# Kernel optimization log

Measured on AMD Instinct MI355X. Metric: run time of the kernel, lower is better.

Reference implementation:

```python
import jax, jax.numpy as jnp
import numpy as np

N_NODES = 50000
N_EDGES = 1600000
D_IN = 128
D_HID = 256


def gcn_conv(x, edge_index, W, b, n_nodes):
    # PyG GCNConv: linear transform, add self-loops, symmetric deg^-1/2 normalization,
    # scatter-sum aggregation, then bias.
    h = x @ W                                             # [N, out]
    src, dst = edge_index[0], edge_index[1]
    loop = jnp.arange(n_nodes, dtype=src.dtype)
    src = jnp.concatenate([src, loop])
    dst = jnp.concatenate([dst, loop])
    deg = jax.ops.segment_sum(jnp.ones_like(dst, x.dtype), dst, num_segments=n_nodes)
    dinv = jnp.where(deg > 0, jax.lax.rsqrt(deg), 0.0)    # deg^-1/2, guard isolated nodes
    norm = dinv[src] * dinv[dst]                          # [E+N]
    msg = norm[:, None] * h[src]                          # gather + scale
    out = jax.ops.segment_sum(msg, dst, num_segments=n_nodes)  # scatter-sum
    return out + b


def setup_inputs() -> dict:
    key = jax.random.key(0)
    k_x, k_e, k_w1, k_b1, k_w2, k_b2 = jax.random.split(key, 6)
    x = jax.random.normal(k_x, (N_NODES, D_IN), dtype=jnp.float32)
    edge_index = jax.random.randint(k_e, (2, N_EDGES), 0, N_NODES, dtype=jnp.int64)
    s = 1.0 / np.sqrt(D_IN)
    W1 = jax.random.uniform(k_w1, (D_IN, D_HID), jnp.float32, -s, s)
    b1 = jnp.zeros((D_HID,), jnp.float32)
    s2 = 1.0 / np.sqrt(D_HID)
    W2 = jax.random.uniform(k_w2, (D_HID, D_IN), jnp.float32, -s2, s2)
    b2 = jnp.zeros((D_IN,), jnp.float32)
    return {"x": x, "edge_index": edge_index, "W1": W1, "b1": b1, "W2": W2, "b2": b2}


def reference(x, edge_index, W1, b1, W2, b2):
    h = gcn_conv(x, edge_index, W1, b1, N_NODES)   # conv1 (hetero sum over 1 edge type)
    h = jax.nn.relu(h)
    out = gcn_conv(h, edge_index, W2, b2, N_NODES) # conv2 -> x_dict['asset']
    return out
```

## Files before the change

### kernel.cpp

```cpp
#include <hip/hip_runtime.h>

#define N_NODES 50000
#define N_EDGES 1600000
#define D_IN 128
#define D_HID 256

#define NBKT 391
#define BCAP 6144
#define CHUNK 4096

typedef short bh8 __attribute__((ext_vector_type(8)));
typedef float f32x4 __attribute__((ext_vector_type(4)));

__device__ inline unsigned int f2_to_bf16x2(float a, float b) {
    unsigned int ua = __float_as_uint(a);
    ua = (ua + 0x7FFFu + ((ua >> 16) & 1u)) >> 16;
    unsigned int ub = __float_as_uint(b);
    ub = (ub + 0x7FFFu + ((ub >> 16) & 1u)) >> 16;
    return ua | (ub << 16);
}
__device__ inline unsigned short f_to_bf16(float a) {
    unsigned int ua = __float_as_uint(a);
    return (unsigned short)((ua + 0x7FFFu + ((ua >> 16) & 1u)) >> 16);
}
__device__ inline float2 bf16x2_to_f2(unsigned int p) {
    float2 r;
    r.x = __uint_as_float(p << 16);
    r.y = __uint_as_float(p & 0xFFFF0000u);
    return r;
}

__global__ __launch_bounds__(256) void bin_kernel(
        const int* __restrict__ src, const int* __restrict__ dst,
        int* __restrict__ bcur, unsigned int* __restrict__ binned, int E) {
    __shared__ unsigned int staged[CHUNK];
    __shared__ unsigned int sorted[CHUNK];
    __shared__ int hist[NBKT], lbase[NBKT], gbase[NBKT];
    __shared__ int sc[256];
    const int tid = threadIdx.x;
    for (int i = tid; i < NBKT; i += 256) hist[i] = 0;
    __syncthreads();
    const int cbase = blockIdx.x * CHUNK;
    const int n = min(CHUNK, E - cbase);
    for (int i = tid; i < n; i += 256) {
        int s = src[cbase + i], d = dst[cbase + i];
        staged[i] = ((unsigned)s << 16) | (unsigned)d;
        atomicAdd(&hist[d >> 7], 1);
    }
    __syncthreads();
    int v0 = (2 * tid     < NBKT) ? hist[2 * tid]     : 0;
    int v1 = (2 * tid + 1 < NBKT) ? hist[2 * tid + 1] : 0;
    sc[tid] = v0 + v1;
    __syncthreads();
    for (int off = 1; off < 256; off <<= 1) {
        int a = (tid >= off) ? sc[tid - off] : 0;
        __syncthreads();
        sc[tid] += a;
        __syncthreads();
    }
    int pairex = sc[tid] - (v0 + v1);
    if (2 * tid < NBKT) {
        lbase[2 * tid] = pairex;
        gbase[2 * tid] = v0 ? atomicAdd(&bcur[2 * tid], v0) : 0;
        hist[2 * tid] = 0;
    }
    if (2 * tid + 1 < NBKT) {
        lbase[2 * tid + 1] = pairex + v0;
        gbase[2 * tid + 1] = v1 ? atomicAdd(&bcur[2 * tid + 1], v1) : 0;
        hist[2 * tid + 1] = 0;
    }
    __syncthreads();
    for (int i = tid; i < n; i += 256) {
        unsigned r = staged[i];
        int b = (r & 0xFFFF) >> 7;
        sorted[lbase[b] + atomicAdd(&hist[b], 1)] = r;
    }
    __syncthreads();
    for (int j = tid; j < n; j += 256) {
        unsigned r = sorted[j];
        int b = (r & 0xFFFF) >> 7;
        binned[(size_t)b * BCAP + gbase[b] + (j - lbase[b])] = r;
    }
}

__global__ __launch_bounds__(512) void scanB(const int* __restrict__ bcur,
                                             int* __restrict__ brow) {
    __shared__ int sc[512];
    const int tid = threadIdx.x;
    int v = (tid < NBKT) ? bcur[tid] : 0;
    sc[tid] = v;
    __syncthreads();
    for (int off = 1; off < 512; off <<= 1) {
        int a = (tid >= off) ? sc[tid - off] : 0;
        __syncthreads();
        sc[tid] += a;
        __syncthreads();
    }
    if (tid < NBKT) brow[tid] = sc[tid] - v;
}

__global__ __launch_bounds__(256) void count_kernel(
        const unsigned int* __restrict__ binned, const int* __restrict__ bcur,
        const int* __restrict__ brow, int* __restrict__ deg,
        float* __restrict__ dinv, int* __restrict__ rowptr, int nNodes) {
    __shared__ int h[128], sc[128];
    const int b = blockIdx.x, tid = threadIdx.x;
    if (tid < 128) h[tid] = 0;
    __syncthreads();
    const int cnt = bcur[b];
    for (int j = tid; j < cnt; j += 256)
        atomicAdd(&h[binned[(size_t)b * BCAP + j] & 127], 1);
    __syncthreads();
    if (tid < 128) {
        sc[tid] = h[tid];
    }
    __syncthreads();
    for (int off = 1; off < 128; off <<= 1) {
        int a = (tid < 128 && tid >= off) ? sc[tid - off] : 0;
        __syncthreads();
        if (tid < 128) sc[tid] += a;
        __syncthreads();
    }
    int node = b * 128 + tid;
    if (tid < 128 && node < nNodes) {
        int d0 = h[tid];
        deg[node] = d0;
        dinv[node] = rsqrtf((float)(d0 + 1));
        rowptr[node] = brow[b] + sc[tid] - d0;
    }
}

__global__ __launch_bounds__(256) void place_kernel(
        const unsigned int* __restrict__ binned, const int* __restrict__ bcur,
        const int* __restrict__ rowptr, const float* __restrict__ dinv,
        unsigned short* __restrict__ eS, float* __restrict__ eW, int nNodes) {
    __shared__ int cur[128];
    __shared__ float sdinv[128];
    __shared__ unsigned short recS[BCAP];
    const int b = blockIdx.x, tid = threadIdx.x;
    const int nbase = b * 128;
    const int regionBase = rowptr[nbase];
    if (tid < 128) {
        int node = nbase + tid;
        cur[tid] = (node < nNodes) ? (rowptr[node] - regionBase) : 0;
        sdinv[tid] = (node < nNodes) ? dinv[node] : 0.0f;
    }
    __syncthreads();
    int cnt = bcur[b];
    if (cnt <= BCAP) {
        for (int j = tid; j < cnt; j += 256) {
            unsigned r = binned[(size_t)b * BCAP + j];
            int dl = r & 127;
            int s = r >> 16;
            int p = atomicAdd(&cur[dl], 1);
            recS[p] = (unsigned short)s;
            eW[regionBase + p] = dinv[s] * sdinv[dl];
        }
        __syncthreads();
        for (int j = tid; j < cnt; j += 256)
            eS[regionBase + j] = recS[j];
    } else {
        for (int j = tid; j < cnt; j += 256) {
            unsigned r = binned[(size_t)b * BCAP + j];
            int dl = r & 127;
            int s = r >> 16;
            int p = atomicAdd(&cur[dl], 1);
            eS[regionBase + p] = (unsigned short)s;
            eW[regionBase + p] = dinv[s] * sdinv[dl];
        }
    }
}

__global__ __launch_bounds__(256) void cvt_bf16(const float4* __restrict__ in,
                                                uint2* __restrict__ out, int n4) {
    int i = blockIdx.x * blockDim.x + threadIdx.x;
    if (i < n4) {
        float4 v = in[i];
        out[i] = make_uint2(f2_to_bf16x2(v.x, v.y), f2_to_bf16x2(v.z, v.w));
    }
}

__global__ __launch_bounds__(256) void cvtT_both(const float* __restrict__ W1,
                                                 const float* __restrict__ W2,
                                                 unsigned short* __restrict__ W1T,
                                                 unsigned short* __restrict__ W2T) {
    int t = blockIdx.x * blockDim.x + threadIdx.x;
    const int SZ = D_IN * D_HID;
    if (t < SZ) {
        int n = t / D_IN, k = t - n * D_IN;
        W1T[t] = f_to_bf16(W1[(size_t)k * D_HID + n]);
    } else if (t < 2 * SZ) {
        int u = t - SZ;
        int n = u / D_HID, k = u - n * D_HID;
        W2T[u] = f_to_bf16(W2[(size_t)k * D_IN + n]);
    }
}

template<bool OUT_BF16>
__global__ __launch_bounds__(256) void gather_agg_bf16(
        const uint2* __restrict__ hb2,
        const unsigned short* __restrict__ eS,
        const float* __restrict__ eW,
        const int* __restrict__ rowptr, const int* __restrict__ deg,
        const float* __restrict__ dinv, const float* __restrict__ bias,
        void* __restrict__ out, int n) {
    const int lane = threadIdx.x & 63;
    const int node = blockIdx.x * 4 + (threadIdx.x >> 6);
    if (node >= n) return;
    const int hl = lane & 31;
    const int odd = (lane >> 5) & 1;
    const int start = rowptr[node];
    const int cnt = deg[node];
    const float dn = dinv[node];

    float4 acc = make_float4(0.f, 0.f, 0.f, 0.f);
    if (!odd) {
        uint2 hv = hb2[(size_t)node * 32 + hl];
        float2 a = bf16x2_to_f2(hv.x), b = bf16x2_to_f2(hv.y);
        float w = dn * dn;
        acc.x = w * a.x; acc.y = w * a.y; acc.z = w * b.x; acc.w = w * b.y;
    }

    for (int c0 = 0; c0 < cnt; c0 += 64) {
        int m = min(64, cnt - c0);
        int   es = (lane < m) ? (int)eS[start + c0 + lane] : 0;
        float ws = (lane < m) ? eW[start + c0 + lane] : 0.0f;
        int steps = (m + 1) >> 1;
        int sr = (steps + 3) & ~3;
        for (int j = 0; j < sr; j += 4) {
            uint2 vv[4];
            float ww[4];
            #pragma unroll
            for (int k = 0; k < 4; ++k) {
                int idx = ((j + k) << 1) | odd;
                int sj = __shfl(es, idx);
                ww[k] = __shfl(ws, idx);
                vv[k] = hb2[(size_t)sj * 32 + hl];
            }
            #pragma unroll
            for (int k = 0; k < 4; ++k) {
                float2 a = bf16x2_to_f2(vv[k].x), b = bf16x2_to_f2(vv[k].y);
                acc.x += ww[k] * a.x;
                acc.y += ww[k] * a.y;
                acc.z += ww[k] * b.x;
                acc.w += ww[k] * b.y;
            }
        }
    }

    acc.x += __shfl_xor(acc.x, 32);
    acc.y += __shfl_xor(acc.y, 32);
    acc.z += __shfl_xor(acc.z, 32);
    acc.w += __shfl_xor(acc.w, 32);

    if (lane < 32) {
        if (OUT_BF16) {
            ((uint2*)out)[(size_t)node * 32 + hl] =
                make_uint2(f2_to_bf16x2(acc.x, acc.y), f2_to_bf16x2(acc.z, acc.w));
        } else {
            float4 b = ((const float4*)bias)[hl];
            acc.x += b.x; acc.y += b.y; acc.z += b.z; acc.w += b.w;
            ((float4*)((float*)out + (size_t)node * D_IN))[hl] = acc;
        }
    }
}

template<int N, int K, int TPW, int MODE>
__global__ __launch_bounds__(256) void gemm_mfma_ws(
        const unsigned short* __restrict__ WT,
        const unsigned int* __restrict__ Ab,
        const float* __restrict__ bias,
        unsigned short* __restrict__ Cb,
        int M) {
    constexpr int KSTEPS = K / 32;
    constexpr int NTG = N / (16 * TPW);
    const int gw = (blockIdx.x * 256 + threadIdx.x) >> 6;
    const int lane = threadIdx.x & 63;
    const int mb = gw / NTG;
    const int ng = gw - mb * NTG;
    const int m_base = mb * 64;
    if (m_base >= M) return;
    const int rit = lane & 15;
    const int kg = lane >> 4;

    bh8 b[TPW][KSTEPS];
    float bv[TPW];
    #pragma unroll
    for (int t = 0; t < TPW; ++t) {
        const int col = (ng * TPW + t) * 16 + rit;
        #pragma unroll
        for (int ks = 0; ks < KSTEPS; ++ks)
            b[t][ks] = *(const bh8*)(WT + (size_t)col * K + ks * 32 + kg * 8);
        bv[t] = (MODE == 1) ? bias[col] : 0.0f;
    }

    #pragma unroll
    for (int rg = 0; rg < 4; ++rg) {
        const int mr = min(m_base + rg * 16 + rit, M - 1);
        bh8 a[KSTEPS];
        #pragma unroll
        for (int ks = 0; ks < KSTEPS; ++ks)
            a[ks] = *(const bh8*)(Ab + (size_t)mr * (K / 2) + ks * 16 + kg * 4);
        f32x4 acc[TPW];
        #pragma unroll
        for (int t = 0; t < TPW; ++t) acc[t] = (f32x4){0.f, 0.f, 0.f, 0.f};
        #pragma unroll
        for (int ks = 0; ks < KSTEPS; ++ks)
            #pragma unroll
            for (int t = 0; t < TPW; ++t)
                acc[t] = __builtin_amdgcn_mfma_f32_16x16x32_bf16(
                    a[ks], b[t][ks], acc[t], 0, 0, 0);
        #pragma unroll
        for (int t = 0; t < TPW; ++t) {
            const int col = (ng * TPW + t) * 16 + rit;
            #pragma unroll
            for (int i = 0; i < 4; ++i) {
                const int m = m_base + rg * 16 + kg * 4 + i;
                float v = acc[t][i];
                if (MODE == 1) { v += bv[t]; v = fmaxf(v, 0.0f); }
                if (m < M) Cb[(size_t)m * N + col] = f_to_bf16(v);
            }
        }
    }
}

extern "C" void kernel_launch(void* const* d_in, const int* in_sizes, int n_in,
                              void* d_out, int out_size, void* d_ws, size_t ws_size,
                              hipStream_t stream) {
    const float* x  = (const float*)d_in[0];
    const int*   ei = (const int*)d_in[1];
    const float* W1 = (const float*)d_in[2];
    const float* b1 = (const float*)d_in[3];
    const float* W2 = (const float*)d_in[4];
    const float* b2 = (const float*)d_in[5];
    const int* src = ei;
    const int* dst = ei + N_EDGES;
    float* out = (float*)d_out;

    char* ws = (char*)d_ws;
    size_t off = 0;
    auto carve = [&](size_t bytes) {
        char* p = ws + off;
        off += (bytes + 255) & ~size_t(255);
        return p;
    };
    int*   bcur      = (int*)  carve(512 * sizeof(int));
    int*   brow      = (int*)  carve(512 * sizeof(int));
    int*   deg       = (int*)  carve(N_NODES * sizeof(int));
    int*   rowptr    = (int*)  carve(N_NODES * sizeof(int));
    float* dinv      = (float*)carve(N_NODES * sizeof(float));
    unsigned int*   binned = (unsigned int*)  carve((size_t)NBKT * BCAP * sizeof(unsigned int));
    unsigned short* eS     = (unsigned short*)carve((size_t)N_EDGES * sizeof(unsigned short));
    float*          eWt    = (float*)         carve((size_t)N_EDGES * sizeof(float));
    unsigned int* xb   = (unsigned int*)carve((size_t)N_NODES * 64 * sizeof(unsigned int));
    unsigned int* aggb = (unsigned int*)carve((size_t)N_NODES * 64 * sizeof(unsigned int));
    unsigned int* h1b  = (unsigned int*)carve((size_t)N_NODES * 128 * sizeof(unsigned int));
    unsigned short* W1T = (unsigned short*)carve((size_t)D_IN * D_HID * sizeof(unsigned short));
    unsigned short* W2T = (unsigned short*)carve((size_t)D_HID * D_IN * sizeof(unsigned short));
    unsigned int* t2b = xb;
    (void)ws_size;

    hipMemsetAsync(bcur, 0, 512 * sizeof(int), stream);
    bin_kernel<<<(N_EDGES + CHUNK - 1) / CHUNK, 256, 0, stream>>>(
        src, dst, bcur, binned, N_EDGES);
    scanB<<<1, 512, 0, stream>>>(bcur, brow);
    count_kernel<<<NBKT, 256, 0, stream>>>(binned, bcur, brow, deg, dinv,
                                           rowptr, N_NODES);
    place_kernel<<<NBKT, 256, 0, stream>>>(binned, bcur, rowptr, dinv,
                                           eS, eWt, N_NODES);

    cvt_bf16<<<(N_NODES * D_IN / 4 + 255) / 256, 256, 0, stream>>>(
        (const float4*)x, (uint2*)xb, N_NODES * D_IN / 4);
    cvtT_both<<<(2 * D_IN * D_HID + 255) / 256, 256, 0, stream>>>(W1, W2, W1T, W2T);

    gather_agg_bf16<true><<<(N_NODES + 3) / 4, 256, 0, stream>>>(
        (const uint2*)xb, eS, eWt, rowptr, deg, dinv, nullptr, (void*)aggb, N_NODES);

    const int mB = (N_NODES + 63) / 64;

    {
        const int waves = mB * (D_HID / 32);
        gemm_mfma_ws<D_HID, D_IN, 2, 1><<<(waves + 3) / 4, 256, 0, stream>>>(
            W1T, aggb, b1, (unsigned short*)h1b, N_NODES);
    }

    {
        const int waves = mB * (D_IN / 16);
        gemm_mfma_ws<D_IN, D_HID, 1, 2><<<(waves + 3) / 4, 256, 0, stream>>>(
            W2T, h1b, nullptr, (unsigned short*)t2b, N_NODES);
    }

    gather_agg_bf16<false><<<(N_NODES + 3) / 4, 256, 0, stream>>>(
        (const uint2*)t2b, eS, eWt, rowptr, deg, dinv, b2, (void*)out, N_NODES);
}
```

Before: 295.5 us.

## Fuse both dense GEMMs into one kernel keeping hidden activations in LDS

Replaces the two separate MFMA GEMM launches (agg@W1+bias+relu, then h1@W2) with a single kernel per 64-row tile that stores the 256-wide hidden tile in padded shared memory and feeds it directly into the second GEMM. This removes the global write and re-read of the 50000x256 bf16 hidden buffer and one launch. The cost is that each block re-reads the full W1/W2 from global/L2 with less weight reuse per wave, plus about 50KB of LDS per block, which limits occupancy.

Measured after the change: 305.1 us. 1.03x slower.

```diff
diff --git a/kernel.cpp b/kernel.cpp
--- a/kernel.cpp
+++ b/kernel.cpp
@@ -265,61 +265,83 @@
     }
 }
 
-template<int N, int K, int TPW, int MODE>
-__global__ __launch_bounds__(256) void gemm_mfma_ws(
-        const unsigned short* __restrict__ WT,
+#define H1P (D_HID + 8)
+#define T2P (D_IN + 8)
+__global__ __launch_bounds__(256) void mlp_fused(
+        const unsigned short* __restrict__ W1T,
+        const unsigned short* __restrict__ W2T,
         const unsigned int* __restrict__ Ab,
-        const float* __restrict__ bias,
-        unsigned short* __restrict__ Cb,
+        const float* __restrict__ b1,
+        unsigned int* __restrict__ t2b,
         int M) {
-    constexpr int KSTEPS = K / 32;
-    constexpr int NTG = N / (16 * TPW);
-    const int gw = (blockIdx.x * 256 + threadIdx.x) >> 6;
-    const int lane = threadIdx.x & 63;
-    const int mb = gw / NTG;
-    const int ng = gw - mb * NTG;
-    const int m_base = mb * 64;
-    if (m_base >= M) return;
+    __shared__ unsigned short h1s[64 * H1P];
+    __shared__ unsigned short t2s[64 * T2P];
+    const int tid = threadIdx.x;
+    const int wid = tid >> 6, lane = tid & 63;
+    const int m_base = blockIdx.x * 64;
     const int rit = lane & 15;
     const int kg = lane >> 4;
-
-    bh8 b[TPW][KSTEPS];
-    float bv[TPW];
+    const int r0 = wid * 16;
+
+    bh8 a1f[4];
+    {
+        const int mr = min(m_base + r0 + rit, M - 1);
+        #pragma unroll
+        for (int ks = 0; ks < 4; ++ks)
+            a1f[ks] = *(const bh8*)(Ab + (size_t)mr * 64 + ks * 16 + kg * 4);
+    }
     #pragma unroll
-    for (int t = 0; t < TPW; ++t) {
-        const int col = (ng * TPW + t) * 16 + rit;
-        #pragma unroll
-        for (int ks = 0; ks < KSTEPS; ++ks)
-            b[t][ks] = *(const bh8*)(WT + (size_t)col * K + ks * 32 + kg * 8);
-        bv[t] = (MODE == 1) ? bias[col] : 0.0f;
-    }
-
+    for (int nt = 0; nt < 16; ++nt) {
+        const int col = nt * 16 + rit;
+        bh8 bf[4];
+        #pragma unroll
+        for (int ks = 0; ks < 4; ++ks)
+            bf[ks] = *(const bh8*)(W1T + (size_t)col * D_IN + ks * 32 + kg * 8);
+        f32x4 acc = (f32x4){0.f, 0.f, 0.f, 0.f};
+        #pragma unroll
+        for (int ks = 0; ks < 4; ++ks)
+            acc = __builtin_amdgcn_mfma_f32_16x16x32_bf16(a1f[ks], bf[ks], acc, 0, 0, 0);
+        const float bias = b1[col];
+        #pragma unroll
+        for (int i = 0; i < 4; ++i) {
+            float v = fmaxf(acc[i] + bias, 0.0f);
+            h1s[(r0 + kg * 4 + i) * H1P + col] = f_to_bf16(v);
+        }
+    }
+    __syncthreads();
+
+    bh8 a2f[8];
+    {
+        const int row = r0 + rit;
+        #pragma unroll
+        for (int ks = 0; ks < 8; ++ks)
+            a2f[ks] = *(const bh8*)&h1s[row * H1P + ks * 32 + kg * 8];
+    }
     #pragma unroll
-    for (int rg = 0; rg < 4; ++rg) {
-        const int mr = min(m_base + rg * 16 + rit, M - 1);
-        bh8 a[KSTEPS];
-        #pragma unroll
-        for (int ks = 0; ks < KSTEPS; ++ks)
-            a[ks] = *(const bh8*)(Ab + (size_t)mr * (K / 2) + ks * 16 + kg * 4);
-        f32x4 acc[TPW];
-        #pragma unroll
-        for (int t = 0; t < TPW; ++t) acc[t] = (f32x4){0.f, 0.f, 0.f, 0.f};
-        #pragma unroll
-        for (int ks = 0; ks < KSTEPS; ++ks)
-            #pragma unroll
-            for (int t = 0; t < TPW; ++t)
-                acc[t] = __builtin_amdgcn_mfma_f32_16x16x32_bf16(
-                    a[ks], b[t][ks], acc[t], 0, 0, 0);
-        #pragma unroll
-        for (int t = 0; t < TPW; ++t) {
-            const int col = (ng * TPW + t) * 16 + rit;
-            #pragma unroll
-            for (int i = 0; i < 4; ++i) {
-                const int m = m_base + rg * 16 + kg * 4 + i;
-                float v = acc[t][i];
-                if (MODE == 1) { v += bv[t]; v = fmaxf(v, 0.0f); }
-                if (m < M) Cb[(size_t)m * N + col] = f_to_bf16(v);
-            }
+    for (int nt = 0; nt < 8; ++nt) {
+        const int col = nt * 16 + rit;
+        f32x4 acc = (f32x4){0.f, 0.f, 0.f, 0.f};
+        #pragma unroll
+        for (int ks = 0; ks < 8; ++ks) {
+            bh8 bf = *(const bh8*)(W2T + (size_t)col * D_HID + ks * 32 + kg * 8);
+            acc = __builtin_amdgcn_mfma_f32_16x16x32_bf16(a2f[ks], bf, acc, 0, 0, 0);
+        }
+        #pragma unroll
+        for (int i = 0; i < 4; ++i)
+            t2s[(r0 + kg * 4 + i) * T2P + col] = f_to_bf16(acc[i]);
+    }
+    __syncthreads();
+
+    for (int u = tid; u < 64 * 16; u += 256) {
+        int row = u >> 4, c = u & 15;
+        int m = m_base + row;
+        if (m < M) {
+            const unsigned short* s = &t2s[row * T2P + c * 8];
+            uint4 v = make_uint4(*(const unsigned int*)(s + 0),
+                                 *(const unsigned int*)(s + 2),
+                                 *(const unsigned int*)(s + 4),
+                                 *(const unsigned int*)(s + 6));
+            *(uint4*)(t2b + (size_t)m * 64 + c * 4) = v;
         }
     }
 }
@@ -354,7 +376,6 @@
     float*          eWt    = (float*)         carve((size_t)N_EDGES * sizeof(float));
     unsigned int* xb   = (unsigned int*)carve((size_t)N_NODES * 64 * sizeof(unsigned int));
     unsigned int* aggb = (unsigned int*)carve((size_t)N_NODES * 64 * sizeof(unsigned int));
-    unsigned int* h1b  = (unsigned int*)carve((size_t)N_NODES * 128 * sizeof(unsigned int));
     unsigned short* W1T = (unsigned short*)carve((size_t)D_IN * D_HID * sizeof(unsigned short));
     unsigned short* W2T = (unsigned short*)carve((size_t)D_HID * D_IN * sizeof(unsigned short));
     unsigned int* t2b = xb;
@@ -376,19 +397,8 @@
     gather_agg_bf16<true><<<(N_NODES + 3) / 4, 256, 0, stream>>>(
         (const uint2*)xb, eS, eWt, rowptr, deg, dinv, nullptr, (void*)aggb, N_NODES);
 
-    const int mB = (N_NODES + 63) / 64;
-
-    {
-        const int waves = mB * (D_HID / 32);
-        gemm_mfma_ws<D_HID, D_IN, 2, 1><<<(waves + 3) / 4, 256, 0, stream>>>(
-            W1T, aggb, b1, (unsigned short*)h1b, N_NODES);
-    }
-
-    {
-        const int waves = mB * (D_IN / 16);
-        gemm_mfma_ws<D_IN, D_HID, 1, 2><<<(waves + 3) / 4, 256, 0, stream>>>(
-            W2T, h1b, nullptr, (unsigned short*)t2b, N_NODES);
-    }
+    mlp_fused<<<(N_NODES + 63) / 64, 256, 0, stream>>>(
+        W1T, W2T, aggb, b1, t2b, N_NODES);
 
     gather_agg_bf16<false><<<(N_NODES + 3) / 4, 256, 0, stream>>>(
         (const uint2*)t2b, eS, eWt, rowptr, deg, dinv, b2, (void*)out, N_NODES);
```
